# Performance work log

Measured on AMD Instinct MI355X. Metric: run time of the kernel, lower is better.

The kernel has to match this reference:

```python
import jax, jax.numpy as jnp
import numpy as np

B, S, D, H = 4, 2048, 1024, 16
DH = D // H


def setup_inputs() -> dict:
    key = jax.random.key(0)
    ks = jax.random.split(key, 5)
    std = 1.0 / np.sqrt(D)
    return {
        "x": jax.random.normal(ks[0], (B, S, D), dtype=jnp.float32),
        "mask": jnp.ones((S, S), dtype=bool),  # unused by the original forward
        "Wq": jax.random.normal(ks[1], (D, D), dtype=jnp.float32) * std,
        "Wk": jax.random.normal(ks[2], (D, D), dtype=jnp.float32) * std,
        "Wv": jax.random.normal(ks[3], (D, D), dtype=jnp.float32) * std,
        "Wout": jax.random.normal(ks[4], (D, D), dtype=jnp.float32) * std,
    }


def reference(x, mask, Wq, Wk, Wv, Wout):
    n, s, d = x.shape
    scale = 1.0 / np.sqrt(DH).astype(np.float32)
    q = (x @ Wq).reshape(n, s, H, DH)
    k = (x @ Wk).reshape(n, s, H, DH)
    v = (x @ Wv).reshape(n, s, H, DH)
    # scores [n, q, k, h]; softmax over k axis (dim=-2 in original)
    attn = jnp.einsum('nqhd,nkhd->nqkh', q, k) * scale
    attn = jax.nn.softmax(attn, axis=-2)
    z = jnp.einsum('nqkh,nkhd->nqhd', attn, v).reshape(n, s, d)
    z = jnp.einsum('nqd,de->nqe', z, Wout)
    return x + z
```

## Files before the change

### kernel.cpp

```cpp
#include <hip/hip_runtime.h>

#define Bn 4
#define Sn 2048
#define Dn 1024
#define Hn 16
#define DHn 64

typedef float f32x4 __attribute__((ext_vector_type(4)));
typedef short bf16x8 __attribute__((ext_vector_type(8)));
typedef unsigned short u16;
typedef unsigned int u32;
typedef unsigned short u16x8 __attribute__((ext_vector_type(8)));
typedef unsigned short u16x4 __attribute__((ext_vector_type(4)));
typedef u32 u32x4 __attribute__((ext_vector_type(4)));

union B8 { u32x4 u; bf16x8 s; u16x8 h; };

__device__ __forceinline__ u16 f2bf(float f){
  union { float f; u32 u; } v; v.f = f;
  return (u16)((v.u + 0x7fffu + ((v.u >> 16) & 1u)) >> 16);
}

__device__ __forceinline__ u32 pack_bf2(float lo, float hi){
  union { float f; u32 u; } a, b;
  a.f = lo; b.f = hi;
  return __builtin_amdgcn_perm(b.u, a.u, 0x07060302u);
}

#if __has_builtin(__builtin_amdgcn_exp2f)
#define EXP2(x) __builtin_amdgcn_exp2f(x)
#define QSCALE 0.18033688011112042f
#else
#define EXP2(x) __expf(x)
#define QSCALE 0.125f
#endif

#if __has_builtin(__builtin_amdgcn_global_load_lds)
#define G2L16(l, g) __builtin_amdgcn_global_load_lds((const __attribute__((address_space(1))) u32*)(g), \
                                                     (__attribute__((address_space(3))) u32*)(l), 16, 0, 0)
#else
#define G2L16(l, g) (*(bf16x8*)(l) = *(const bf16x8*)(g))
#endif

#define MFMA_B16(d, va, vb) (d) = __builtin_amdgcn_mfma_f32_16x16x32_bf16((va), (vb), (d), 0, 0, 0)
#define BARRAW() __builtin_amdgcn_s_barrier()
#define WAIT_LGKM0() asm volatile("s_waitcnt lgkmcnt(0)" ::: "memory")
#define VM4() asm volatile("s_waitcnt vmcnt(4)" ::: "memory")
#define VM0() asm volatile("s_waitcnt vmcnt(0)" ::: "memory")
#define SCHEDB() __builtin_amdgcn_sched_barrier(0)

__global__ void prep_kernel(const float* __restrict__ x,
                            const float* __restrict__ Wq, const float* __restrict__ Wk,
                            const float* __restrict__ Wv, const float* __restrict__ Wo,
                            u16* __restrict__ xb, u16* __restrict__ wt_all){
  __shared__ u16 tile[64*66];
  const int t = threadIdx.x;
  if (blockIdx.x < 4096){
    size_t i = ((size_t)blockIdx.x * 256 + t) * 8;
    float4 f0 = *(const float4*)(x + i);
    float4 f1 = *(const float4*)(x + i + 4);
    u16x8 o;
    o[0]=f2bf(f0.x); o[1]=f2bf(f0.y); o[2]=f2bf(f0.z); o[3]=f2bf(f0.w);
    o[4]=f2bf(f1.x); o[5]=f2bf(f1.y); o[6]=f2bf(f1.z); o[7]=f2bf(f1.w);
    *(u16x8*)(xb + i) = o;
    return;
  }
  const int wi = blockIdx.x - 4096;
  const int z = wi >> 8, r8 = wi & 255;
  const int k0 = (r8 >> 4) * 64, n0 = (r8 & 15) * 64;
  const float* w = (z == 0) ? Wq : (z == 1) ? Wk : (z == 2) ? Wv : Wo;
  const float scale = (z == 0) ? QSCALE : 1.0f;
  u16* wt = wt_all + (size_t)z * Dn * Dn;
  #pragma unroll
  for (int i = 0; i < 4; i++){
    int idx = i*256 + t;
    int r = idx >> 4, c4 = (idx & 15) * 4;
    float4 f = *(const float4*)(w + (size_t)(k0 + r)*Dn + n0 + c4);
    tile[r*66 + c4 + 0] = f2bf(f.x * scale);
    tile[r*66 + c4 + 1] = f2bf(f.y * scale);
    tile[r*66 + c4 + 2] = f2bf(f.z * scale);
    tile[r*66 + c4 + 3] = f2bf(f.w * scale);
  }
  __syncthreads();
  #pragma unroll
  for (int i = 0; i < 4; i++){
    int idx = i*256 + t;
    int nr = idx >> 4, kc4 = (idx & 15) * 4;
    u16x4 o;
    o[0] = tile[(kc4+0)*66 + nr];
    o[1] = tile[(kc4+1)*66 + nr];
    o[2] = tile[(kc4+2)*66 + nr];
    o[3] = tile[(kc4+3)*66 + nr];
    *(u16x4*)(wt + (size_t)(n0 + nr)*Dn + k0 + kc4) = o;
  }
}

__launch_bounds__(256)
__global__ void gemm_qkv_kernel(const u16* __restrict__ xb, const u16* __restrict__ wt_all,
                                u16* __restrict__ qb, u16* __restrict__ kb, u16* __restrict__ vtb){
  __shared__ u16 sm[40960];
  const int t = threadIdx.x;
  const int lane = t & 63, wave = t >> 6;
  const int ln = lane & 15, quad = lane >> 4;
  const int wm = wave >> 1, wn = wave & 1;

  const int lin = blockIdx.x;
  const int wg = (lin & 7) * 192 + (lin >> 3);
  const int zsel = wg >> 9;
  const int rem = wg & 511;
  const int m0 = (rem >> 3) * 128;
  const int n0 = (rem & 7) * 128;
  const u16* wt = wt_all + (size_t)zsel * Dn * Dn;

  const u16* ap[4]; const u16* bp[4]; int ldo[4];
  #pragma unroll
  for (int p = 0; p < 4; p++){
    int idx = p*256 + t;
    int r = idx >> 3, g = (idx & 7) ^ (r & 7);
    ap[p] = xb + (size_t)(m0 + r)*Dn + g*8;
    bp[p] = wt + (size_t)(n0 + r)*Dn + g*8;
    ldo[p] = idx * 8;
  }
#define STGA(buf, tt) do { _Pragma("unroll") for (int p = 0; p < 4; p++) \
    G2L16(&sm[(buf) + ldo[p]], ap[p] + (size_t)(tt)*64); } while(0)
#define STGB(buf, tt) do { _Pragma("unroll") for (int p = 0; p < 4; p++) \
    G2L16(&sm[(buf) + ldo[p]], bp[p] + (size_t)(tt)*64); } while(0)

  const int agr0 = ((    quad) ^ (ln & 7)) * 8;
  const int agr1 = ((4 + quad) ^ (ln & 7)) * 8;
  int arow[4], brow[4];
  #pragma unroll
  for (int i = 0; i < 4; i++) arow[i] = (wm*64 + i*16 + ln) * 64;
  #pragma unroll
  for (int j = 0; j < 4; j++) brow[j] = (wn*64 + j*16 + ln) * 64;

  f32x4 acc[4][4] = {};

  STGA(0, 0); STGB(24576, 0); STGA(8192, 1);

  #pragma unroll
  for (int tt = 0; tt < 16; ++tt){
    const int a_cur = (tt % 3) * 8192;
    const int a_pf  = ((tt + 2) % 3) * 8192;
    const int b_cur = 24576 + (tt & 1) * 8192;
    const int b_pf  = 24576 + ((tt + 1) & 1) * 8192;

    if (tt < 15) { VM4(); } else { VM0(); }
    BARRAW(); SCHEDB();

    bf16x8 a01[2][2], bq[4][2];
    #pragma unroll
    for (int i = 0; i < 2; i++){
      a01[i][0] = *(const bf16x8*)&sm[a_cur + arow[i] + agr0];
      a01[i][1] = *(const bf16x8*)&sm[a_cur + arow[i] + agr1];
    }
    #pragma unroll
    for (int j = 0; j < 4; j++){
      bq[j][0] = *(const bf16x8*)&sm[b_cur + brow[j] + agr0];
      bq[j][1] = *(const bf16x8*)&sm[b_cur + brow[j] + agr1];
    }
    SCHEDB();
    if (tt < 15) STGB(b_pf, tt + 1);
    SCHEDB();
    WAIT_LGKM0(); SCHEDB();
    __builtin_amdgcn_s_setprio(1);
    #pragma unroll
    for (int i = 0; i < 2; i++)
      #pragma unroll
      for (int j = 0; j < 4; j++){
        MFMA_B16(acc[i][j], a01[i][0], bq[j][0]);
        MFMA_B16(acc[i][j], a01[i][1], bq[j][1]);
      }
    __builtin_amdgcn_s_setprio(0);

    bf16x8 a23[2][2];
    #pragma unroll
    for (int i = 0; i < 2; i++){
      a23[i][0] = *(const bf16x8*)&sm[a_cur + arow[2+i] + agr0];
      a23[i][1] = *(const bf16x8*)&sm[a_cur + arow[2+i] + agr1];
    }
    SCHEDB();
    if (tt < 14) STGA(a_pf, tt + 2);
    SCHEDB();
    WAIT_LGKM0(); SCHEDB();
    __builtin_amdgcn_s_setprio(1);
    #pragma unroll
    for (int i = 0; i < 2; i++)
      #pragma unroll
      for (int j = 0; j < 4; j++){
        MFMA_B16(acc[2+i][j], a23[i][0], bq[j][0]);
        MFMA_B16(acc[2+i][j], a23[i][1], bq[j][1]);
      }
    __builtin_amdgcn_s_setprio(0);
  }

  __syncthreads();
  u16* Cs = sm;
  if (zsel < 2){
    u16* outp = (zsel == 0) ? qb : kb;
    #pragma unroll
    for (int rb = 0; rb < 4; rb++)
      #pragma unroll
      for (int cb = 0; cb < 4; cb++)
        #pragma unroll
        for (int reg = 0; reg < 4; reg++)
          Cs[(wm*64 + rb*16 + quad*4 + reg)*136 + wn*64 + cb*16 + ln] = f2bf(acc[rb][cb][reg]);
    __syncthreads();
    #pragma unroll
    for (int i = 0; i < 8; i++){
      int idx = i*256 + t;
      int r = idx >> 4, c8 = (idx & 15) * 8;
      bf16x8 vdat = *(const bf16x8*)&Cs[r*136 + c8];
      int row = m0 + r, bb = row >> 11, s = row & 2047;
      int col = n0 + c8, hh = col >> 6, d = col & 63;
      *(bf16x8*)(outp + (((size_t)bb*Hn + hh)*Sn + s)*DHn + d) = vdat;
    }
  } else {
    #pragma unroll
    for (int rb = 0; rb < 4; rb++)
      #pragma unroll
      for (int cb = 0; cb < 4; cb++){
        u16x4 o;
        #pragma unroll
        for (int reg = 0; reg < 4; reg++) o[reg] = f2bf(acc[rb][cb][reg]);
        *(u16x4*)&Cs[(wn*64 + cb*16 + ln)*136 + wm*64 + rb*16 + quad*4] = o;
      }
    __syncthreads();
    #pragma unroll
    for (int i = 0; i < 8; i++){
      int idx = i*256 + t;
      int c = idx >> 4, r8 = (idx & 15) * 8;
      bf16x8 vdat = *(const bf16x8*)&Cs[c*136 + r8];
      int col = n0 + c, hh = col >> 6, d = col & 63;
      int row = m0 + r8, bb = row >> 11, s = row & 2047;
      *(bf16x8*)(vtb + (((size_t)bb*Hn + hh)*DHn + d)*Sn + s) = vdat;
    }
  }
#undef STGA
#undef STGB
}

__launch_bounds__(512, 4)
__global__ void attn_kernel(const u16* q, const u16* __restrict__ k,
                            const u16* __restrict__ vt, u16* z){
  __shared__ u16 Ks[2][64*64];
  __shared__ u16 Vs[2][64*64];
  const int t = threadIdx.x;
  const int wave = t >> 6, lane = t & 63;
  const int ln = lane & 15, quad = lane >> 4;
  const int lin = blockIdx.x + 8*(blockIdx.y + 16*blockIdx.z);
  const int wgs = (lin & 7)*64 + (lin >> 3);
  const int qt = wgs & 7, h = (wgs >> 3) & 15, b = wgs >> 7;
  const size_t bh = (size_t)b * Hn + h;
  const int q0 = qt*256 + wave*32;
  const u16* qp = q + bh * Sn * DHn;
  const u16* kp = k + bh * Sn * DHn;
  const u16* vp = vt + bh * DHn * Sn;

  bf16x8 qf[2][2];
  #pragma unroll
  for (int n = 0; n < 2; n++)
    #pragma unroll
    for (int kq = 0; kq < 2; kq++)
      qf[n][kq] = *(const bf16x8*)(qp + (size_t)(q0 + n*16 + ln)*DHn + kq*32 + quad*8);

  f32x4 zacc[4][2] = {};
  float dacc[2] = {0.f, 0.f};

  const int r = t >> 3, a = t & 7;
  const int ksg = a >> 2, q1 = ((a&3)*2)&3, h1 = (a&3) >> 1;
  const int vc1 = ksg*32 + q1*8 + h1*4;
  const int vc2 = ksg*32 + (((q1+1)&3))*8 + h1*4;
  const int kpos  = r*64 + (a ^ (r&7))*8;
  const int vpos1 = r*64 + ((vc1>>3) ^ (r&7))*8 + (vc1 & 7);
  const int vpos2 = r*64 + ((vc2>>3) ^ (r&7))*8 + (vc2 & 7);

  bf16x8 rk, rv;
  rk = *(const bf16x8*)(kp + (size_t)r*DHn + a*8);
  rv = *(const bf16x8*)(vp + (size_t)r*Sn + a*8);
  {
    *(bf16x8*)&Ks[0][kpos] = rk;
    u16x4 lo = *(u16x4*)&rv;
    u16x4 hi = *((u16x4*)&rv + 1);
    *(u16x4*)&Vs[0][vpos1] = lo;
    *(u16x4*)&Vs[0][vpos2] = hi;
  }

  const int kg0 = ((    quad) ^ (ln & 7)) * 8;
  const int kg1 = ((4 + quad) ^ (ln & 7)) * 8;

  for (int kt = 0; kt < Sn/64; kt++){
    const int cur = kt & 1;
    __syncthreads();

    if (kt + 1 < Sn/64){
      rk = *(const bf16x8*)(kp + (size_t)((kt+1)*64 + r)*DHn + a*8);
      rv = *(const bf16x8*)(vp + (size_t)r*Sn + (kt+1)*64 + a*8);
    }
    const u16* Kc = Ks[cur];
    const u16* Vc = Vs[cur];

    #pragma unroll
    for (int ks = 0; ks < 2; ks++){
      f32x4 sacc[2][2] = {};
      #pragma unroll
      for (int kq = 0; kq < 2; kq++){
        const int kgo = kq ? kg1 : kg0;
        bf16x8 ka[2];
        #pragma unroll
        for (int m2 = 0; m2 < 2; m2++)
          ka[m2] = *(const bf16x8*)&Kc[((2*ks + m2)*16 + ln)*64 + kgo];
        #pragma unroll
        for (int m2 = 0; m2 < 2; m2++)
          #pragma unroll
          for (int n = 0; n < 2; n++)
            sacc[m2][n] = __builtin_amdgcn_mfma_f32_16x16x32_bf16(ka[m2], qf[n][kq], sacc[m2][n], 0, 0, 0);
      }
      B8 pb[2];
      #pragma unroll
      for (int n = 0; n < 2; n++){
        f32x4 s0 = sacc[0][n], s1 = sacc[1][n];
        float a0 = EXP2(s0[0]), a1 = EXP2(s0[1]), a2 = EXP2(s0[2]), a3 = EXP2(s0[3]);
        float b0 = EXP2(s1[0]), b1 = EXP2(s1[1]), b2 = EXP2(s1[2]), b3 = EXP2(s1[3]);
        dacc[n] += ((a0 + a1) + (a2 + a3)) + ((b0 + b1) + (b2 + b3));
        pb[n].u = (u32x4){pack_bf2(a0, a1), pack_bf2(a2, a3), pack_bf2(b0, b1), pack_bf2(b2, b3)};
      }
      const int vgo = ks ? kg1 : kg0;
      #pragma unroll
      for (int mtd = 0; mtd < 4; mtd++){
        bf16x8 va = *(const bf16x8*)&Vc[(mtd*16 + ln)*64 + vgo];
        #pragma unroll
        for (int n = 0; n < 2; n++)
          zacc[mtd][n] = __builtin_amdgcn_mfma_f32_16x16x32_bf16(va, pb[n].s, zacc[mtd][n], 0, 0, 0);
      }
    }

    if (kt + 1 < Sn/64){
      const int nxt = (kt+1) & 1;
      *(bf16x8*)&Ks[nxt][kpos] = rk;
      u16x4 lo = *(u16x4*)&rv;
      u16x4 hi = *((u16x4*)&rv + 1);
      *(u16x4*)&Vs[nxt][vpos1] = lo;
      *(u16x4*)&Vs[nxt][vpos2] = hi;
    }
  }

  float inv[2];
  #pragma unroll
  for (int n = 0; n < 2; n++){
    float d = dacc[n];
    d += __shfl_xor(d, 16, 64);
    d += __shfl_xor(d, 32, 64);
    inv[n] = 1.0f / d;
  }

  #pragma unroll
  for (int mtd = 0; mtd < 4; mtd++)
    #pragma unroll
    for (int n = 0; n < 2; n++){
      u16x4 o;
      #pragma unroll
      for (int j = 0; j < 4; j++) o[j] = f2bf(zacc[mtd][n][j] * inv[n]);
      *(u16x4*)(z + (bh*Sn + (size_t)(q0 + n*16 + ln))*DHn + mtd*16 + quad*4) = o;
    }
}

__launch_bounds__(256)
__global__ void gemm_out_kernel(const u16* __restrict__ zb, const u16* __restrict__ wt,
                                const float* __restrict__ x, float* __restrict__ out){
  __shared__ u16 sm[40960];
  const int t = threadIdx.x;
  const int lane = t & 63, wave = t >> 6;
  const int ln = lane & 15, quad = lane >> 4;
  const int wm = wave >> 1, wn = wave & 1;

  const int lin = blockIdx.x;
  const int wg = (lin & 7) * 64 + (lin >> 3);
  const int m0 = (wg >> 3) * 128;
  const int n0 = (wg & 7) * 128;

  const u16* ap[4]; const u16* bp[4]; int ldo[4];
  #pragma unroll
  for (int p = 0; p < 4; p++){
    int idx = p*256 + t;
    int r = idx >> 3, g = (idx & 7) ^ (r & 7);
    int row = m0 + r, bb = row >> 11, s = row & 2047;
    ap[p] = zb + ((size_t)bb*Hn*Sn + s)*DHn + g*8;
    bp[p] = wt + (size_t)(n0 + r)*Dn + g*8;
    ldo[p] = idx * 8;
  }
#define STGA(buf, tt) do { _Pragma("unroll") for (int p = 0; p < 4; p++) \
    G2L16(&sm[(buf) + ldo[p]], ap[p] + (size_t)(tt)*Sn*DHn); } while(0)
#define STGB(buf, tt) do { _Pragma("unroll") for (int p = 0; p < 4; p++) \
    G2L16(&sm[(buf) + ldo[p]], bp[p] + (size_t)(tt)*64); } while(0)

  const int agr0 = ((    quad) ^ (ln & 7)) * 8;
  const int agr1 = ((4 + quad) ^ (ln & 7)) * 8;
  int arow[4], brow[4];
  #pragma unroll
  for (int i = 0; i < 4; i++) arow[i] = (wm*64 + i*16 + ln) * 64;
  #pragma unroll
  for (int j = 0; j < 4; j++) brow[j] = (wn*64 + j*16 + ln) * 64;

  f32x4 acc[4][4] = {};
  STGA(0, 0); STGB(24576, 0); STGA(8192, 1);

  #pragma unroll
  for (int tt = 0; tt < 16; ++tt){
    const int a_cur = (tt % 3) * 8192;
    const int a_pf  = ((tt + 2) % 3) * 8192;
    const int b_cur = 24576 + (tt & 1) * 8192;
    const int b_pf  = 24576 + ((tt + 1) & 1) * 8192;

    if (tt < 15) { VM4(); } else { VM0(); }
    BARRAW(); SCHEDB();

    bf16x8 a01[2][2], bq[4][2];
    #pragma unroll
    for (int i = 0; i < 2; i++){
      a01[i][0] = *(const bf16x8*)&sm[a_cur + arow[i] + agr0];
      a01[i][1] = *(const bf16x8*)&sm[a_cur + arow[i] + agr1];
    }
    #pragma unroll
    for (int j = 0; j < 4; j++){
      bq[j][0] = *(const bf16x8*)&sm[b_cur + brow[j] + agr0];
      bq[j][1] = *(const bf16x8*)&sm[b_cur + brow[j] + agr1];
    }
    SCHEDB();
    if (tt < 15) STGB(b_pf, tt + 1);
    SCHEDB();
    WAIT_LGKM0(); SCHEDB();
    __builtin_amdgcn_s_setprio(1);
    #pragma unroll
    for (int i = 0; i < 2; i++)
      #pragma unroll
      for (int j = 0; j < 4; j++){
        MFMA_B16(acc[i][j], a01[i][0], bq[j][0]);
        MFMA_B16(acc[i][j], a01[i][1], bq[j][1]);
      }
    __builtin_amdgcn_s_setprio(0);

    bf16x8 a23[2][2];
    #pragma unroll
    for (int i = 0; i < 2; i++){
      a23[i][0] = *(const bf16x8*)&sm[a_cur + arow[2+i] + agr0];
      a23[i][1] = *(const bf16x8*)&sm[a_cur + arow[2+i] + agr1];
    }
    SCHEDB();
    if (tt < 14) STGA(a_pf, tt + 2);
    SCHEDB();
    WAIT_LGKM0(); SCHEDB();
    __builtin_amdgcn_s_setprio(1);
    #pragma unroll
    for (int i = 0; i < 2; i++)
      #pragma unroll
      for (int j = 0; j < 4; j++){
        MFMA_B16(acc[2+i][j], a23[i][0], bq[j][0]);
        MFMA_B16(acc[2+i][j], a23[i][1], bq[j][1]);
      }
    __builtin_amdgcn_s_setprio(0);
  }

  #pragma unroll
  for (int rb = 0; rb < 4; rb++)
    #pragma unroll
    for (int cb = 0; cb < 4; cb++)
      #pragma unroll
      for (int reg = 0; reg < 4; reg++){
        int row = m0 + wm*64 + rb*16 + quad*4 + reg;
        int col = n0 + wn*64 + cb*16 + ln;
        size_t off = (size_t)row*Dn + col;
        out[off] = acc[rb][cb][reg] + x[off];
      }
#undef STGA
#undef STGB
}

extern "C" void kernel_launch(void* const* d_in, const int* in_sizes, int n_in,
                              void* d_out, int out_size, void* d_ws, size_t ws_size,
                              hipStream_t stream){
  const float* x    = (const float*)d_in[0];
  const float* Wq   = (const float*)d_in[2];
  const float* Wk   = (const float*)d_in[3];
  const float* Wv   = (const float*)d_in[4];
  const float* Wout = (const float*)d_in[5];
  float* out = (float*)d_out;

  u16* ws = (u16*)d_ws;
  const size_t NW = (size_t)Dn * Dn;
  const size_t NX = (size_t)Bn * Sn * Dn;
  u16* wt  = ws;
  u16* xb  = wt + 4*NW;
  u16* qb  = xb + NX;
  u16* kb  = qb + NX;
  u16* vtb = kb + NX;

  prep_kernel     <<<dim3(4096 + 1024), dim3(256), 0, stream>>>(x, Wq, Wk, Wv, Wout, xb, wt);
  gemm_qkv_kernel <<<dim3(1536), dim3(256), 0, stream>>>(xb, wt, qb, kb, vtb);
  attn_kernel     <<<dim3(8,16,4), dim3(512), 0, stream>>>(qb, kb, vtb, qb);
  gemm_out_kernel <<<dim3(512), dim3(256), 0, stream>>>(qb, wt + 3*NW, x, out);
}
```

Before: 252.9 us.

## Stream K tiles directly to LDS with four-deep buffering and deeper V prefetch

The attention loop now loads K tiles with global_load_lds straight into a 4-slot LDS ring, with the XOR swizzle moved to the global address side. V is prefetched two tiles ahead through a pair of register buffers. Synchronisation uses explicit vmcnt/lgkmcnt waits and a single raw barrier per tile. MFMA groups are wrapped in s_setprio to favour matrix issue. The aim is to hide global-load latency and drop the register round-trip for K, at the cost of 16KB more LDS per block, which may reduce how many blocks fit per CU.

Result: slower. 568.1 us (+124.7%).

```diff
diff --git a/kernel.cpp b/kernel.cpp
--- a/kernel.cpp
+++ b/kernel.cpp
@@ -46,6 +46,7 @@
 #define BARRAW() __builtin_amdgcn_s_barrier()
 #define WAIT_LGKM0() asm volatile("s_waitcnt lgkmcnt(0)" ::: "memory")
 #define VM4() asm volatile("s_waitcnt vmcnt(4)" ::: "memory")
+#define VM2() asm volatile("s_waitcnt vmcnt(2)" ::: "memory")
 #define VM0() asm volatile("s_waitcnt vmcnt(0)" ::: "memory")
 #define SCHEDB() __builtin_amdgcn_sched_barrier(0)
 
@@ -243,7 +244,7 @@
 __launch_bounds__(512, 4)
 __global__ void attn_kernel(const u16* q, const u16* __restrict__ k,
                             const u16* __restrict__ vt, u16* z){
-  __shared__ u16 Ks[2][64*64];
+  __shared__ u16 Ks[4][64*64];
   __shared__ u16 Vs[2][64*64];
   const int t = threadIdx.x;
   const int wave = t >> 6, lane = t & 63;
@@ -268,82 +269,99 @@
   float dacc[2] = {0.f, 0.f};
 
   const int r = t >> 3, a = t & 7;
+  const u16* kgp = kp + (size_t)r*DHn + ((a ^ (r & 7)) * 8);
+  const int kldo = t * 8;
+#define STGK(buf, tt) G2L16(&Ks[buf][kldo], kgp + (size_t)(tt)*4096)
   const int ksg = a >> 2, q1 = ((a&3)*2)&3, h1 = (a&3) >> 1;
   const int vc1 = ksg*32 + q1*8 + h1*4;
   const int vc2 = ksg*32 + (((q1+1)&3))*8 + h1*4;
-  const int kpos  = r*64 + (a ^ (r&7))*8;
   const int vpos1 = r*64 + ((vc1>>3) ^ (r&7))*8 + (vc1 & 7);
   const int vpos2 = r*64 + ((vc2>>3) ^ (r&7))*8 + (vc2 & 7);
-
-  bf16x8 rk, rv;
-  rk = *(const bf16x8*)(kp + (size_t)r*DHn + a*8);
-  rv = *(const bf16x8*)(vp + (size_t)r*Sn + a*8);
+  const u16* vgp = vp + (size_t)r*Sn + a*8;
+
+  const int kg0 = ((    quad) ^ (ln & 7)) * 8;
+  const int kg1 = ((4 + quad) ^ (ln & 7)) * 8;
+
+  bf16x8 rvbuf[2];
+  STGK(0, 0);
+  rvbuf[0] = *(const bf16x8*)(vgp);
+  STGK(1, 1);
+  rvbuf[1] = *(const bf16x8*)(vgp + 64);
+  VM2();
   {
-    *(bf16x8*)&Ks[0][kpos] = rk;
-    u16x4 lo = *(u16x4*)&rv;
-    u16x4 hi = *((u16x4*)&rv + 1);
+    u16x4 lo = *(u16x4*)&rvbuf[0];
+    u16x4 hi = *((u16x4*)&rvbuf[0] + 1);
     *(u16x4*)&Vs[0][vpos1] = lo;
     *(u16x4*)&Vs[0][vpos2] = hi;
   }
-
-  const int kg0 = ((    quad) ^ (ln & 7)) * 8;
-  const int kg1 = ((4 + quad) ^ (ln & 7)) * 8;
-
-  for (int kt = 0; kt < Sn/64; kt++){
-    const int cur = kt & 1;
-    __syncthreads();
-
-    if (kt + 1 < Sn/64){
-      rk = *(const bf16x8*)(kp + (size_t)((kt+1)*64 + r)*DHn + a*8);
-      rv = *(const bf16x8*)(vp + (size_t)r*Sn + (kt+1)*64 + a*8);
-    }
-    const u16* Kc = Ks[cur];
-    const u16* Vc = Vs[cur];
-
-    #pragma unroll
-    for (int ks = 0; ks < 2; ks++){
-      f32x4 sacc[2][2] = {};
-      #pragma unroll
-      for (int kq = 0; kq < 2; kq++){
-        const int kgo = kq ? kg1 : kg0;
-        bf16x8 ka[2];
+  WAIT_LGKM0();
+  BARRAW();
+
+  for (int ko = 0; ko < 8; ++ko){
+    #pragma unroll
+    for (int ku = 0; ku < 4; ++ku){
+      const int kt = ko*4 + ku;
+
+      if (kt < 30){
+        STGK((ku+2)&3, kt+2);
+        rvbuf[ku&1] = *(const bf16x8*)(vgp + (kt+2)*64);
+        SCHEDB();
+      }
+
+      const u16* Kc = Ks[ku & 3];
+      const u16* Vc = Vs[ku & 1];
+
+      #pragma unroll
+      for (int ks = 0; ks < 2; ks++){
+        f32x4 sacc[2][2] = {};
         #pragma unroll
-        for (int m2 = 0; m2 < 2; m2++)
-          ka[m2] = *(const bf16x8*)&Kc[((2*ks + m2)*16 + ln)*64 + kgo];
+        for (int kq = 0; kq < 2; kq++){
+          const int kgo = kq ? kg1 : kg0;
+          bf16x8 ka[2];
+          #pragma unroll
+          for (int m2 = 0; m2 < 2; m2++)
+            ka[m2] = *(const bf16x8*)&Kc[((2*ks + m2)*16 + ln)*64 + kgo];
+          __builtin_amdgcn_s_setprio(1);
+          #pragma unroll
+          for (int m2 = 0; m2 < 2; m2++)
+            #pragma unroll
+            for (int n = 0; n < 2; n++)
+              sacc[m2][n] = __builtin_amdgcn_mfma_f32_16x16x32_bf16(ka[m2], qf[n][kq], sacc[m2][n], 0, 0, 0);
+          __builtin_amdgcn_s_setprio(0);
+        }
+        B8 pb[2];
         #pragma unroll
-        for (int m2 = 0; m2 < 2; m2++)
+        for (int n = 0; n < 2; n++){
+          f32x4 s0 = sacc[0][n], s1 = sacc[1][n];
+          float a0 = EXP2(s0[0]), a1 = EXP2(s0[1]), a2 = EXP2(s0[2]), a3 = EXP2(s0[3]);
+          float b0 = EXP2(s1[0]), b1 = EXP2(s1[1]), b2 = EXP2(s1[2]), b3 = EXP2(s1[3]);
+          dacc[n] += ((a0 + a1) + (a2 + a3)) + ((b0 + b1) + (b2 + b3));
+          pb[n].u = (u32x4){pack_bf2(a0, a1), pack_bf2(a2, a3), pack_bf2(b0, b1), pack_bf2(b2, b3)};
+        }
+        const int vgo = ks ? kg1 : kg0;
+        #pragma unroll
+        for (int mtd = 0; mtd < 4; mtd++){
+          bf16x8 va = *(const bf16x8*)&Vc[(mtd*16 + ln)*64 + vgo];
+          __builtin_amdgcn_s_setprio(1);
           #pragma unroll
           for (int n = 0; n < 2; n++)
-            sacc[m2][n] = __builtin_amdgcn_mfma_f32_16x16x32_bf16(ka[m2], qf[n][kq], sacc[m2][n], 0, 0, 0);
-      }
-      B8 pb[2];
-      #pragma unroll
-      for (int n = 0; n < 2; n++){
-        f32x4 s0 = sacc[0][n], s1 = sacc[1][n];
-        float a0 = EXP2(s0[0]), a1 = EXP2(s0[1]), a2 = EXP2(s0[2]), a3 = EXP2(s0[3]);
-        float b0 = EXP2(s1[0]), b1 = EXP2(s1[1]), b2 = EXP2(s1[2]), b3 = EXP2(s1[3]);
-        dacc[n] += ((a0 + a1) + (a2 + a3)) + ((b0 + b1) + (b2 + b3));
-        pb[n].u = (u32x4){pack_bf2(a0, a1), pack_bf2(a2, a3), pack_bf2(b0, b1), pack_bf2(b2, b3)};
-      }
-      const int vgo = ks ? kg1 : kg0;
-      #pragma unroll
-      for (int mtd = 0; mtd < 4; mtd++){
-        bf16x8 va = *(const bf16x8*)&Vc[(mtd*16 + ln)*64 + vgo];
-        #pragma unroll
-        for (int n = 0; n < 2; n++)
-          zacc[mtd][n] = __builtin_amdgcn_mfma_f32_16x16x32_bf16(va, pb[n].s, zacc[mtd][n], 0, 0, 0);
-      }
-    }
-
-    if (kt + 1 < Sn/64){
-      const int nxt = (kt+1) & 1;
-      *(bf16x8*)&Ks[nxt][kpos] = rk;
-      u16x4 lo = *(u16x4*)&rv;
-      u16x4 hi = *((u16x4*)&rv + 1);
-      *(u16x4*)&Vs[nxt][vpos1] = lo;
-      *(u16x4*)&Vs[nxt][vpos2] = hi;
-    }
-  }
+            zacc[mtd][n] = __builtin_amdgcn_mfma_f32_16x16x32_bf16(va, pb[n].s, zacc[mtd][n], 0, 0, 0);
+          __builtin_amdgcn_s_setprio(0);
+        }
+      }
+
+      if (kt < 31){
+        if (kt < 30) { VM2(); } else { VM0(); }
+        u16x4 lo = *(u16x4*)&rvbuf[(ku+1)&1];
+        u16x4 hi = *((u16x4*)&rvbuf[(ku+1)&1] + 1);
+        *(u16x4*)&Vs[(ku+1)&1][vpos1] = lo;
+        *(u16x4*)&Vs[(ku+1)&1][vpos2] = hi;
+        WAIT_LGKM0();
+        BARRAW();
+      }
+    }
+  }
+#undef STGK
 
   float inv[2];
   #pragma unroll
```
